# Kernel tuning notes

Hardware: AMD Instinct MI355X
Metric: run time of the kernel (lower is better)

Reference implementation:

```python
import jax, jax.numpy as jnp
import numpy as np

B, T, E, H, V, C = 64, 1024, 256, 512, 30522, 2


def setup_inputs() -> dict:
    key = jax.random.key(0)
    ks = jax.random.split(key, 20)
    tokens = jax.random.randint(ks[0], (B, T), 0, V, dtype=jnp.int32)
    emb = jax.random.normal(ks[1], (V, E), dtype=jnp.float32) * 0.02
    def lin(k, out_d, in_d, bias_const=0.0):
        W = jax.random.normal(k, (out_d, in_d), dtype=jnp.float32) / np.sqrt(in_d)
        b = jnp.full((out_d,), bias_const, dtype=jnp.float32)
        return W, b
    # layer 0: input E, layer 1: input H
    Wr0, br0 = lin(ks[2], H, E + H)
    Wz0, bz0 = lin(ks[3], H, E + H, -2.0)
    Wh0, bh0 = lin(ks[4], H, E + H)
    Wr1, br1 = lin(ks[5], H, H + H)
    Wz1, bz1 = lin(ks[6], H, H + H, -2.0)
    Wh1, bh1 = lin(ks[7], H, H + H)
    fcW, fcb = lin(ks[8], C, H)
    return dict(tokens=tokens, emb=emb,
                Wr0=Wr0, br0=br0, Wz0=Wz0, bz0=bz0, Wh0=Wh0, bh0=bh0,
                Wr1=Wr1, br1=br1, Wz1=Wz1, bz1=bz1, Wh1=Wh1, bh1=bh1,
                fcW=fcW, fcb=fcb)


def _run_layer(xs, Wr, br, Wz, bz, Wh, bh):
    # xs: [B, T, D_in]. Weight layout [H, D_in + H] as torch Linear on cat([x, h]).
    D = xs.shape[-1]
    Wrx, Wrh = Wr[:, :D], Wr[:, D:]
    Wzx, Wzh = Wz[:, :D], Wz[:, D:]
    Whx, Whh = Wh[:, :D], Wh[:, D:]
    # Precompute input contributions for all timesteps (same math as per-step cat).
    xr = jnp.einsum('btd,hd->bth', xs, Wrx) + br
    xz = jnp.einsum('btd,hd->bth', xs, Wzx) + bz
    xh = jnp.einsum('btd,hd->bth', xs, Whx) + bh
    def step(h, inp):
        xr_t, xz_t, xh_t = inp
        r = jax.nn.sigmoid(xr_t + h @ Wrh.T)
        z = jax.nn.sigmoid(xz_t + h @ Wzh.T)
        h_tilde = jnp.tanh(xh_t + (r * h) @ Whh.T)
        h_new = (1.0 - z) * h + z * h_tilde
        return h_new, h_new
    h0 = jnp.zeros((xs.shape[0], Wr.shape[0]), dtype=xs.dtype)
    # time-major for scan
    seq = (xr.transpose(1, 0, 2), xz.transpose(1, 0, 2), xh.transpose(1, 0, 2))
    h_last, hs = jax.lax.scan(step, h0, seq)
    return hs.transpose(1, 0, 2), h_last  # [B,T,H], [B,H]


def reference(tokens, emb, Wr0, br0, Wz0, bz0, Wh0, bh0,
              Wr1, br1, Wz1, bz1, Wh1, bh1, fcW, fcb):
    x = emb[tokens]  # [B, T, E]
    hs0, _ = _run_layer(x, Wr0, br0, Wz0, bz0, Wh0, bh0)
    _, h_last = _run_layer(hs0, Wr1, br1, Wz1, bz1, Wh1, bh1)
    return h_last @ fcW.T + fcb  # [B, C]
```

## Files before the change

### kernel.cpp

```cpp
#include <hip/hip_runtime.h>
#include <math.h>

#define H0A_OFF  0
#define H0B_OFF  32768
#define H1_OFF   65536
#define RH0_OFF  98304
#define RH1_OFF  131072
#define FLG_OFF  163840
#define WS_FLOATS (163840 + 512)
#define WS_BYTES  (WS_FLOATS * 4)

#define SROW 516

__device__ __forceinline__ void gstore(float* p, float v) {
    __hip_atomic_store(p, v, __ATOMIC_RELAXED, __HIP_MEMORY_SCOPE_AGENT);
}
__device__ __forceinline__ unsigned gloadU(const unsigned* p) {
    return __hip_atomic_load(p, __ATOMIC_RELAXED, __HIP_MEMORY_SCOPE_AGENT);
}
__device__ __forceinline__ void gstoreU(unsigned* p, unsigned v) {
    __hip_atomic_store(p, v, __ATOMIC_RELAXED, __HIP_MEMORY_SCOPE_AGENT);
}
__device__ __forceinline__ float fma4(float4 w, float4 x, float a) {
    a = fmaf(w.x, x.x, a); a = fmaf(w.y, x.y, a);
    a = fmaf(w.z, x.z, a); a = fmaf(w.w, x.w, a);
    return a;
}

__device__ __forceinline__ void issueSlice(float4 t[8], const float* __restrict__ src,
                                           int lane, int cbase) {
    #pragma unroll
    for (int i = 0; i < 8; ++i) {
        int f4i = lane + 64 * i, rowL = f4i >> 4, c4 = f4i & 15;
        const float* p = src + rowL * 512 + cbase + 4 * c4;
        asm volatile("global_load_dwordx4 %0, %1, off sc0 sc1"
                     : "=&v"(t[i]) : "v"(p) : "memory");
    }
}
__device__ __forceinline__ void writeSlice(float* __restrict__ buf, const float4 t[8],
                                           int lane, int cbase) {
    #pragma unroll
    for (int i = 0; i < 8; ++i) {
        int f4i = lane + 64 * i, rowL = f4i >> 4, c4 = f4i & 15;
        *(float4*)&buf[rowL * SROW + cbase + 4 * c4] = t[i];
    }
}
__device__ __forceinline__ void drain_all() {
    asm volatile("s_waitcnt vmcnt(0)" ::: "memory");
}
__device__ __forceinline__ void drain_keep8() {
    asm volatile("s_waitcnt vmcnt(8)" ::: "memory");
}

__device__ __forceinline__ void gbar(unsigned* arrD, unsigned* goOwn,
                                     const unsigned* goOth, int myIdx, bool agg,
                                     int tid, unsigned tag, unsigned otag) {
    __syncthreads();
    if (agg) {
        if (tid < 64) {
            if (tid == 0) gstoreU(arrD + myIdx, tag);
            for (;;) {
                bool ok = ((int)(gloadU(arrD + tid) - tag) >= 0) &&
                          ((int)(gloadU(goOth) - otag) >= 0);
                if (__ballot(ok) == ~0ull) break;
                __builtin_amdgcn_s_sleep(2);
            }
            if (tid == 0) gstoreU(goOwn, tag);
        }
    } else if (tid == 0) {
        gstoreU(arrD + myIdx, tag);
        while ((int)(gloadU(goOwn) - tag) < 0)
            __builtin_amdgcn_s_sleep(2);
    }
    __syncthreads();
}

__global__ __launch_bounds__(512, 1) void gru_main(
    const int* __restrict__ tokens, const float* __restrict__ emb,
    const float* __restrict__ Wr0, const float* __restrict__ br0,
    const float* __restrict__ Wz0, const float* __restrict__ bz0,
    const float* __restrict__ Wh0, const float* __restrict__ bh0,
    const float* __restrict__ Wr1, const float* __restrict__ br1,
    const float* __restrict__ Wz1, const float* __restrict__ bz1,
    const float* __restrict__ Wh1, const float* __restrict__ bh1,
    float* __restrict__ ws)
{
    const int blk = blockIdx.x;
    const int tid = threadIdx.x;

    const int rg    = (blk >> 2) & 1;
    const int jl    = blk & 3;
    const int jh    = (blk >> 3) & 15;
    const int layer = blk >> 7;
    const int j     = jh * 4 + jl;
    const int ks    = tid >> 6;
    const int lane  = tid & 63;
    const int c     = lane >> 3;
    const int rgl   = lane & 7;
    const int rowbase = rg * 32;
    const int cg    = j * 8 + c;
    const int cR    = (tid >> 5) & 7;
    const int riR   = tid & 31;
    const int cgR   = j * 8 + cR;

    unsigned* flg  = (unsigned*)(ws + FLG_OFF);
    const int dom  = layer * 2 + rg;
    const int odom = (layer ? 0 : 2) + rg;
    unsigned* arrD  = flg + dom * 64;
    unsigned* goOwn = flg + 256 + dom * 16;
    unsigned* goOth = flg + 256 + odom * 16;
    const bool agg  = (j == 0);

    const int S1 = layer ? 512 : 256;
    const int K  = S1 + 512;
    const float* WrL = layer ? Wr1 : Wr0;
    const float* WzL = layer ? Wz1 : Wz0;
    const float* WhL = layer ? Wh1 : Wh0;
    const float* wrRow = WrL + (size_t)cg * K;
    const float* wzRow = WzL + (size_t)cg * K;
    const float* whRow = WhL + (size_t)cg * K;
    const float bR = (layer ? br1 : br0)[cgR];
    const float bZ = (layer ? bz1 : bz0)[cgR];
    const float bH = (layer ? bh1 : bh0)[cgR];

    const float* h0buf[2] = { ws + H0A_OFF, ws + H0B_OFF };
    float* h0bufW[2] = { ws + H0A_OFF, ws + H0B_OFF };
    float* h1p   = ws + H1_OFF;
    float* rhOwn = ws + (layer ? RH1_OFF : RH0_OFF);

    __shared__ float bufA[32 * SROW];
    __shared__ float bufB[32 * SROW];
    __shared__ float pTmp[3 * 2048];

    const int k1     = ks * (S1 >> 3);
    const int k2s    = ks * 64;
    const int k2base = S1 + k2s;
    const int nq1    = S1 >> 5;

    for (int s = 0; s <= 1024; ++s) {
        const bool act = layer ? (s >= 1) : (s < 1024);
        float zv = 0.f, hp = 0.f, hx = 0.f;
        float aR[4] = {0,0,0,0}, aZ[4] = {0,0,0,0}, aH[4] = {0,0,0,0};

        if (act) {
            const float* hReadP = layer ? (const float*)h1p : h0buf[(s - 1) & 1];
            float4 thp[8];
            if (layer) {
                float4 tx[8];
                issueSlice(tx, h0buf[(s - 1) & 1] + rowbase * 512, lane, k1);
                issueSlice(thp, hReadP + rowbase * 512, lane, k2s);
                drain_keep8();
                writeSlice(bufA, tx, lane, k1);
            } else {
                float4 tx[4];
                #pragma unroll
                for (int i = 0; i < 4; ++i) {
                    int f4i = lane + 64 * i, rowL = f4i >> 3, c4 = f4i & 7;
                    int tok = tokens[(rowbase + rowL) * 1024 + s];
                    tx[i] = *(const float4*)(emb + (size_t)tok * 256 + k1 + 4 * c4);
                }
                issueSlice(thp, hReadP + rowbase * 512, lane, k2s);
                drain_keep8();
                #pragma unroll
                for (int i = 0; i < 4; ++i) {
                    int f4i = lane + 64 * i, rowL = f4i >> 3, c4 = f4i & 7;
                    *(float4*)&bufA[rowL * SROW + k1 + 4 * c4] = tx[i];
                }
            }

            #pragma unroll 4
            for (int i = 0; i < nq1; ++i) {
                int kk = k1 + 4 * i;
                float4 w1 = *(const float4*)(wrRow + kk);
                float4 w2 = *(const float4*)(wzRow + kk);
                float4 w3 = *(const float4*)(whRow + kk);
                #pragma unroll
                for (int rr = 0; rr < 4; ++rr) {
                    float4 xv = *(const float4*)(&bufA[(rgl + 8 * rr) * SROW + kk]);
                    aR[rr] = fma4(w1, xv, aR[rr]);
                    aZ[rr] = fma4(w2, xv, aZ[rr]);
                    aH[rr] = fma4(w3, xv, aH[rr]);
                }
            }

            drain_all();
            writeSlice(bufB, thp, lane, k2s);

            #pragma unroll 4
            for (int i = 0; i < 16; ++i) {
                int kw  = k2base + 4 * i;
                int kst = k2s + 4 * i;
                float4 w1 = *(const float4*)(wrRow + kw);
                float4 w2 = *(const float4*)(wzRow + kw);
                #pragma unroll
                for (int rr = 0; rr < 4; ++rr) {
                    float4 xv = *(const float4*)(&bufB[(rgl + 8 * rr) * SROW + kst]);
                    aR[rr] = fma4(w1, xv, aR[rr]);
                    aZ[rr] = fma4(w2, xv, aZ[rr]);
                }
            }
            #pragma unroll
            for (int rr = 0; rr < 4; ++rr) {
                int o = ks * 256 + c * 32 + (rgl + 8 * rr);
                pTmp[o]        = aR[rr];
                pTmp[2048 + o] = aZ[rr];
                pTmp[4096 + o] = aH[rr];
            }
        }
        __syncthreads();

        if (act && tid < 256) {
            int o = cR * 32 + riR;
            float sR = 0.f, sZ = 0.f, sH = 0.f;
            #pragma unroll
            for (int p = 0; p < 8; ++p) {
                sR += pTmp[o + 256 * p];
                sZ += pTmp[2048 + o + 256 * p];
                sH += pTmp[4096 + o + 256 * p];
            }
            float rv = 1.f / (1.f + expf(-(sR + bR)));
            zv = 1.f / (1.f + expf(-(sZ + bZ)));
            hx = sH;
            hp = bufB[riR * SROW + cgR];
            gstore(rhOwn + (rowbase + riR) * 512 + cgR, rv * hp);
        }

        gbar(arrD, goOwn, goOth, j, agg, tid, (unsigned)(2 * s + 1),
             (!layer && s >= 2) ? (unsigned)(2 * s - 1) : 0u);

        if (act) {
            float4 trh[8];
            issueSlice(trh, rhOwn + rowbase * 512, lane, k2s);
            drain_all();
            writeSlice(bufB, trh, lane, k2s);
            float a3[4] = {0,0,0,0};
            #pragma unroll 4
            for (int i = 0; i < 16; ++i) {
                int kw  = k2base + 4 * i;
                int kst = k2s + 4 * i;
                float4 w3 = *(const float4*)(whRow + kw);
                #pragma unroll
                for (int rr = 0; rr < 4; ++rr) {
                    float4 xv = *(const float4*)(&bufB[(rgl + 8 * rr) * SROW + kst]);
                    a3[rr] = fma4(w3, xv, a3[rr]);
                }
            }
            #pragma unroll
            for (int rr = 0; rr < 4; ++rr)
                pTmp[ks * 256 + c * 32 + (rgl + 8 * rr)] = a3[rr];
        }
        __syncthreads();

        if (act && tid < 256) {
            float* hWriteP = layer ? h1p : h0bufW[s & 1];
            int o = cR * 32 + riR;
            float sH2 = 0.f;
            #pragma unroll
            for (int p = 0; p < 8; ++p) sH2 += pTmp[o + 256 * p];
            float ht = tanhf(hx + sH2 + bH);
            float hn = (1.f - zv) * hp + zv * ht;
            gstore(hWriteP + (rowbase + riR) * 512 + cgR, hn);
        }

        gbar(arrD, goOwn, goOth, j, agg, tid, (unsigned)(2 * s + 2),
             layer ? (unsigned)(2 * s + 2) : 0u);
    }
}

__global__ __launch_bounds__(128) void gru_fc(
    const float* __restrict__ h1f, const float* __restrict__ fcW,
    const float* __restrict__ fcb, float* __restrict__ out)
{
    int tid = threadIdx.x;
    int b = tid >> 1, cc = tid & 1;
    const float* hrow = h1f + b * 512;
    const float* wrow = fcW + cc * 512;
    float acc = 0.f;
    #pragma unroll 4
    for (int k = 0; k < 512; k += 4) {
        float4 hv = *(const float4*)(hrow + k);
        float4 wv = *(const float4*)(wrow + k);
        acc = fmaf(hv.x, wv.x, fmaf(hv.y, wv.y, fmaf(hv.z, wv.z, fmaf(hv.w, wv.w, acc))));
    }
    out[b * 2 + cc] = acc + fcb[cc];
}

extern "C" void kernel_launch(void* const* d_in, const int* in_sizes, int n_in,
                              void* d_out, int out_size, void* d_ws, size_t ws_size,
                              hipStream_t stream) {
    const int* tokens = (const int*)d_in[0];
    const float* emb = (const float*)d_in[1];
    const float* Wr0 = (const float*)d_in[2];  const float* br0 = (const float*)d_in[3];
    const float* Wz0 = (const float*)d_in[4];  const float* bz0 = (const float*)d_in[5];
    const float* Wh0 = (const float*)d_in[6];  const float* bh0 = (const float*)d_in[7];
    const float* Wr1 = (const float*)d_in[8];  const float* br1 = (const float*)d_in[9];
    const float* Wz1 = (const float*)d_in[10]; const float* bz1 = (const float*)d_in[11];
    const float* Wh1 = (const float*)d_in[12]; const float* bh1 = (const float*)d_in[13];
    const float* fcW = (const float*)d_in[14]; const float* fcb = (const float*)d_in[15];
    float* ws = (float*)d_ws;

    hipMemsetAsync(d_ws, 0, WS_BYTES, stream);

    gru_main<<<256, 512, 0, stream>>>(tokens, emb, Wr0, br0, Wz0, bz0, Wh0, bh0,
                                      Wr1, br1, Wz1, bz1, Wh1, bh1, ws);
    gru_fc<<<1, 128, 0, stream>>>(ws + H1_OFF, fcW, fcb, (float*)d_out);
}
```

Before: 14.72 ms.

## Replace aggregator grid barriers with per-producer flag waits

Removes the two-phase gather/release barrier, which ran through an aggregator block per domain. Each block now publishes per-step flags for its rh and h slices. Each wavefront waits only on the 8 producer blocks whose columns it actually reads, and the cross-layer dependency becomes point-to-point flag checks. This cuts the barrier round-trip latency and lets blocks proceed as soon as their specific inputs are ready, at the cost of more polling traffic and more subtle memory-ordering correctness.

```diff
diff --git a/kernel.cpp b/kernel.cpp
--- a/kernel.cpp
+++ b/kernel.cpp
@@ -7,7 +7,7 @@
 #define RH0_OFF  98304
 #define RH1_OFF  131072
 #define FLG_OFF  163840
-#define WS_FLOATS (163840 + 512)
+#define WS_FLOATS (163840 + 1024)
 #define WS_BYTES  (WS_FLOATS * 4)
 
 #define SROW 516
@@ -52,27 +52,17 @@
     asm volatile("s_waitcnt vmcnt(8)" ::: "memory");
 }
 
-__device__ __forceinline__ void gbar(unsigned* arrD, unsigned* goOwn,
-                                     const unsigned* goOth, int myIdx, bool agg,
-                                     int tid, unsigned tag, unsigned otag) {
-    __syncthreads();
-    if (agg) {
-        if (tid < 64) {
-            if (tid == 0) gstoreU(arrD + myIdx, tag);
-            for (;;) {
-                bool ok = ((int)(gloadU(arrD + tid) - tag) >= 0) &&
-                          ((int)(gloadU(goOth) - otag) >= 0);
-                if (__ballot(ok) == ~0ull) break;
-                __builtin_amdgcn_s_sleep(2);
-            }
-            if (tid == 0) gstoreU(goOwn, tag);
-        }
-    } else if (tid == 0) {
-        gstoreU(arrD + myIdx, tag);
-        while ((int)(gloadU(goOwn) - tag) < 0)
-            __builtin_amdgcn_s_sleep(2);
-    }
-    __syncthreads();
+__device__ __forceinline__ void wait8(const unsigned* F, int base, int skip,
+                                      unsigned tgt, int lane) {
+    for (;;) {
+        bool ok = true;
+        if (lane < 8) {
+            int jj = base + lane;
+            ok = (jj == skip) || ((int)(gloadU(F + jj) - tgt) >= 0);
+        }
+        if (__ballot(ok) == ~0ull) break;
+        __builtin_amdgcn_s_sleep(2);
+    }
 }
 
 __global__ __launch_bounds__(512, 1) void gru_main(
@@ -105,11 +95,12 @@
 
     unsigned* flg  = (unsigned*)(ws + FLG_OFF);
     const int dom  = layer * 2 + rg;
-    const int odom = (layer ? 0 : 2) + rg;
-    unsigned* arrD  = flg + dom * 64;
-    unsigned* goOwn = flg + 256 + dom * 16;
-    unsigned* goOth = flg + 256 + odom * 16;
-    const bool agg  = (j == 0);
+    unsigned* rhF  = flg;
+    unsigned* hF   = flg + 256;
+    unsigned* rhFd = rhF + dom * 64;
+    unsigned* hFd  = hF + dom * 64;
+    unsigned* hFx  = hF + rg * 64;
+    unsigned* rhFo = rhF + (2 + rg) * 64;
 
     const int S1 = layer ? 512 : 256;
     const int K  = S1 + 512;
@@ -143,23 +134,25 @@
         float aR[4] = {0,0,0,0}, aZ[4] = {0,0,0,0}, aH[4] = {0,0,0,0};
 
         if (act) {
-            const float* hReadP = layer ? (const float*)h1p : h0buf[(s - 1) & 1];
             float4 thp[8];
             if (layer) {
                 float4 tx[8];
+                wait8(hFx, 8 * ks, -1, (unsigned)s, lane);
                 issueSlice(tx, h0buf[(s - 1) & 1] + rowbase * 512, lane, k1);
-                issueSlice(thp, hReadP + rowbase * 512, lane, k2s);
+                wait8(hFd, 8 * ks, j, (unsigned)s, lane);
+                issueSlice(thp, h1p + rowbase * 512, lane, k2s);
                 drain_keep8();
                 writeSlice(bufA, tx, lane, k1);
             } else {
                 float4 tx[4];
+                wait8(hFd, 8 * ks, j, (unsigned)s, lane);
                 #pragma unroll
                 for (int i = 0; i < 4; ++i) {
                     int f4i = lane + 64 * i, rowL = f4i >> 3, c4 = f4i & 7;
                     int tok = tokens[(rowbase + rowL) * 1024 + s];
                     tx[i] = *(const float4*)(emb + (size_t)tok * 256 + k1 + 4 * c4);
                 }
-                issueSlice(thp, hReadP + rowbase * 512, lane, k2s);
+                issueSlice(thp, h0buf[(s - 1) & 1] + rowbase * 512, lane, k2s);
                 drain_keep8();
                 #pragma unroll
                 for (int i = 0; i < 4; ++i) {
@@ -224,12 +217,12 @@
             hp = bufB[riR * SROW + cgR];
             gstore(rhOwn + (rowbase + riR) * 512 + cgR, rv * hp);
         }
-
-        gbar(arrD, goOwn, goOth, j, agg, tid, (unsigned)(2 * s + 1),
-             (!layer && s >= 2) ? (unsigned)(2 * s - 1) : 0u);
+        __syncthreads();
+        if (tid == 0) gstoreU(rhFd + j, (unsigned)(s + 1));
 
         if (act) {
             float4 trh[8];
+            wait8(rhFd, 8 * ks, j, (unsigned)(s + 1), lane);
             issueSlice(trh, rhOwn + rowbase * 512, lane, k2s);
             drain_all();
             writeSlice(bufB, trh, lane, k2s);
@@ -252,6 +245,13 @@
         __syncthreads();
 
         if (act && tid < 256) {
+            if (!layer && s >= 2) {
+                for (;;) {
+                    bool ok = ((int)(gloadU(rhFo + lane) - (unsigned)s) >= 0);
+                    if (__ballot(ok) == ~0ull) break;
+                    __builtin_amdgcn_s_sleep(2);
+                }
+            }
             float* hWriteP = layer ? h1p : h0bufW[s & 1];
             int o = cR * 32 + riR;
             float sH2 = 0.f;
@@ -261,9 +261,8 @@
             float hn = (1.f - zv) * hp + zv * ht;
             gstore(hWriteP + (rowbase + riR) * 512 + cgR, hn);
         }
-
-        gbar(arrD, goOwn, goOth, j, agg, tid, (unsigned)(2 * s + 2),
-             layer ? (unsigned)(2 * s + 2) : 0u);
+        __syncthreads();
+        if (tid == 0) gstoreU(hFd + j, (unsigned)(s + 1));
     }
 }
 
```

Result: slower. 23.26 ms (+58.1%).
